# Kernel optimization log

Measured on AMD Instinct MI355X. Metric: run time of the kernel, lower is better.

The kernel has to match this reference:

```python
import jax, jax.numpy as jnp
import numpy as np

NEG_SLOPE = 0.2
EPS = 1e-5


def seg_softmax(e, idx, n):
    # numerically stable segment softmax over segments given by idx
    m = jax.ops.segment_max(e, idx, num_segments=n)
    ex = jnp.exp(e - m[idx])
    s = jax.ops.segment_sum(ex, idx, num_segments=n)
    return ex / (s[idx] + 1e-16)


def seg_mean(v, idx, n):
    s = jax.ops.segment_sum(v, idx, num_segments=n)
    cnt = jax.ops.segment_sum(jnp.ones((v.shape[0],), v.dtype), idx, num_segments=n)
    return s / jnp.maximum(cnt, 1.0)[:, None]


def setup_inputs() -> dict:
    key = jax.random.key(0)
    ks = jax.random.split(key, 20)
    N, E, C, H, G, L = 50000, 400000, 128, 4, 64, 4
    HC, MID = H * C, C * (H // 2)
    s = 0.05
    inp = {
        "x": jax.random.normal(ks[0], (N, C), jnp.float32),
        "edge_index": jax.random.randint(ks[1], (2, E), 0, N),
        "instr_vectors": jax.random.normal(ks[2], (L, G, C), jnp.float32),
        "global_language_feats": jax.random.normal(ks[3], (G, C), jnp.float32),
        "edge_attr": jax.random.normal(ks[4], (E, C), jnp.float32),
        "batch": jnp.sort(jax.random.randint(ks[5], (N,), 0, G)),
        # per-layer GATv2 conv params
        "Wl": s * jax.random.normal(ks[6], (L, C, HC), jnp.float32),
        "Wr": s * jax.random.normal(ks[7], (L, C, HC), jnp.float32),
        "We": s * jax.random.normal(ks[8], (L, C, HC), jnp.float32),
        "att": s * jax.random.normal(ks[9], (L, H, C), jnp.float32),
        # instruction-conditioned node-mask projection
        "Wm": s * jax.random.normal(ks[10], (L, C, C), jnp.float32),
        # x_proj MLP
        "p1_w": s * jax.random.normal(ks[11], (L, HC, MID), jnp.float32),
        "p1_b": jnp.zeros((L, MID), jnp.float32),
        "p2_w": s * jax.random.normal(ks[12], (L, MID, C), jnp.float32),
        "p2_b": jnp.zeros((L, C), jnp.float32),
        # GraphNorm params
        "gn_gamma": jnp.ones((L, C), jnp.float32),
        "gn_beta": jnp.zeros((L, C), jnp.float32),
        "gn_alpha": jnp.ones((L, C), jnp.float32),
    }
    return inp


def reference(x, edge_index, instr_vectors, global_language_feats, edge_attr, batch,
              Wl, Wr, We, att, Wm, p1_w, p1_b, p2_w, p2_b, gn_gamma, gn_beta, gn_alpha):
    N, C = x.shape
    L, G, _ = instr_vectors.shape
    H = att.shape[1]
    src, dst = edge_index[0], edge_index[1]
    inv_sqrt_c = 1.0 / jnp.sqrt(jnp.asarray(C, x.dtype))
    h = x
    for i in range(L):
        instr = instr_vectors[i]  # [G, C]
        # instruction-conditioned soft node mask (interpretable_mode)
        mask = jax.nn.sigmoid(jnp.sum((h @ Wm[i]) * instr[batch], axis=-1, keepdims=True) * inv_sqrt_c)  # [N,1]
        x_in = mask * h
        # GATv2 conv with edge features, heads concatenated
        xl = (x_in @ Wl[i]).reshape(N, H, C)
        xr = (x_in @ Wr[i]).reshape(N, H, C)
        ea = (edge_attr @ We[i]).reshape(-1, H, C)
        m = jax.nn.leaky_relu(xl[src] + xr[dst] + ea, NEG_SLOPE)           # [E,H,C]
        e = jnp.einsum('ehc,hc->eh', m, att[i])                            # [E,H]
        alpha = seg_softmax(e, dst, N)                                     # [E,H]
        out = jax.ops.segment_sum(alpha[:, :, None] * xl[src], dst, num_segments=N)  # [N,H,C]
        out = out.reshape(N, H * C)
        # x_proj MLP
        cr = jax.nn.gelu(out @ p1_w[i] + p1_b[i])
        cr = jax.nn.gelu(cr @ p2_w[i] + p2_b[i])                           # [N,C]
        # scatter scaled-dot-product attention: instruction query gates nodes per graph
        s = jnp.sum(instr[batch] * cr, axis=-1) * inv_sqrt_c               # [N]
        a = seg_softmax(s, batch, G)                                       # [N]
        cr = a[:, None] * cr
        # GraphNorm per graph
        mean = seg_mean(cr, batch, G)                                      # [G,C]
        sub = cr - gn_alpha[i] * mean[batch]
        var = seg_mean(sub * sub, batch, G)                                # [G,C]
        cr = gn_gamma[i] * sub / jnp.sqrt(var[batch] + EPS) + gn_beta[i]
        # residual + interpretable mask gating
        h = mask * (cr + h)
    return h
```

## Files before the change

kernel.cpp:

```cpp
#include <hip/hip_runtime.h>
#include <math.h>

#define CDIV(a,b) (((a)+(b)-1)/(b))

static constexpr int Cc   = 128;
static constexpr int Hh   = 4;
static constexpr int HCc  = 512;
static constexpr int MIDc = 256;
static constexpr float INV_SQRT_C = 0.08838834764831845f;

typedef __attribute__((ext_vector_type(8))) short bf16x8;
typedef __attribute__((ext_vector_type(4))) float f32x4;

__device__ __forceinline__ unsigned short f2bf(float f) {
    unsigned u = __float_as_uint(f);
    unsigned r = (u + 0x7FFFu + ((u >> 16) & 1u)) >> 16;
    return (unsigned short)r;
}
__device__ __forceinline__ float bf2f(unsigned short v) {
    return __uint_as_float(((unsigned)v) << 16);
}

__device__ __forceinline__ float gelu_tanh(float x) {
    float x3 = x * x * x;
    float t = tanhf(0.7978845608028654f * (x + 0.044715f * x3));
    return 0.5f * x * (1.0f + t);
}

__global__ void k_init_gb(int* gbeg, int* gend, int N, int G) {
    int g = blockIdx.x * blockDim.x + threadIdx.x;
    if (g < G) { gbeg[g] = N; gend[g] = 0; }
}

__global__ void k_node_bounds(const int* __restrict__ batch, int* gbeg, int* gend, int N) {
    int n = blockIdx.x * blockDim.x + threadIdx.x;
    if (n < N) { int b = batch[n]; atomicMin(&gbeg[b], n); atomicMax(&gend[b], n + 1); }
}

__global__ void k_hist(const int* __restrict__ dst, int* __restrict__ cnt, int E) {
    int e = blockIdx.x * blockDim.x + threadIdx.x;
    if (e < E) atomicAdd(&cnt[dst[e]], 1);
}

__global__ void k_scan_blocks(const int* __restrict__ cnt, int* __restrict__ excl,
                              int* __restrict__ partials, int N) {
    __shared__ int buf[1024];
    int tid = threadIdx.x;
    int i = blockIdx.x * 1024 + tid;
    int v = (i < N) ? cnt[i] : 0;
    buf[tid] = v; __syncthreads();
    for (int off = 1; off < 1024; off <<= 1) {
        int t = (tid >= off) ? buf[tid - off] : 0;
        __syncthreads();
        buf[tid] += t;
        __syncthreads();
    }
    if (i < N) excl[i] = buf[tid] - v;
    if (tid == 1023) partials[blockIdx.x] = buf[1023];
}

__global__ void k_scan_partials(int* partials, int P) {
    __shared__ int buf[1024];
    int tid = threadIdx.x;
    int v = (tid < P) ? partials[tid] : 0;
    buf[tid] = v; __syncthreads();
    for (int off = 1; off < 1024; off <<= 1) {
        int t = (tid >= off) ? buf[tid - off] : 0;
        __syncthreads();
        buf[tid] += t;
        __syncthreads();
    }
    if (tid < P) partials[tid] = buf[tid] - v;
}

__global__ void k_scan_add(int* __restrict__ rowoff, const int* __restrict__ partials, int N, int E) {
    int i = blockIdx.x * 1024 + threadIdx.x;
    if (i < N) rowoff[i] += partials[blockIdx.x];
    if (i == 0) rowoff[N] = E;
}

__global__ void k_scatter(const int* __restrict__ src, const int* __restrict__ dst,
                          const int* __restrict__ rowoff, int* __restrict__ cursor,
                          int* __restrict__ srcs, int* __restrict__ dsts,
                          int* __restrict__ eids, int E) {
    int e = blockIdx.x * blockDim.x + threadIdx.x;
    if (e < E) {
        int d = dst[e];
        int p = rowoff[d] + atomicAdd(&cursor[d], 1);
        srcs[p] = src[e];
        dsts[p] = d;
        eids[p] = e;
    }
}

__global__ void k_conv_ea(const float* __restrict__ edge_attr, const int* __restrict__ eids,
                          unsigned short* __restrict__ eaT, int E) {
    int idx = blockIdx.x * blockDim.x + threadIdx.x;
    if (idx >= E * 32) return;
    int p = idx >> 5, j = idx & 31;
    int eid = eids[p];
    float4 v = *(const float4*)(edge_attr + (size_t)eid * Cc + j * 4);
    unsigned short o[4] = {f2bf(v.x), f2bf(v.y), f2bf(v.z), f2bf(v.w)};
    *(ushort4*)(eaT + (size_t)p * Cc + j * 4) = *(ushort4*)o;
}

__global__ void k_w2bf_t(const float* __restrict__ W, unsigned short* __restrict__ Wt,
                         int K, int N, int lgK) {
    int total = K * N;
    const float* Wl = W + (size_t)blockIdx.y * total;
    unsigned short* Wo = Wt + (size_t)blockIdx.y * total;
    int idx = blockIdx.x * blockDim.x + threadIdx.x;
    if (idx >= total) return;
    int k = idx & (K - 1);
    int n = idx >> lgK;
    Wo[idx] = f2bf(Wl[(size_t)k * N + n]);
}

__global__ void k_compute_q(const float* __restrict__ Wm, const float* __restrict__ instr,
                            float* __restrict__ q, int G) {
    int idx = blockIdx.x * blockDim.x + threadIdx.x;
    if (idx >= G * Cc) return;
    int g = idx >> 7, k = idx & 127;
    const float* wrow = Wm + (size_t)k * Cc;
    const float* irow = instr + (size_t)g * Cc;
    float acc = 0.f;
    #pragma unroll 8
    for (int j = 0; j < Cc; ++j) acc += wrow[j] * irow[j];
    q[idx] = acc;
}

__global__ __launch_bounds__(256) void k_mask_xin(const float* __restrict__ h,
                                                  const float* __restrict__ q,
                                                  const int* __restrict__ batch,
                                                  float* __restrict__ maskv,
                                                  unsigned short* __restrict__ x_in, int N) {
    int wid = (blockIdx.x * blockDim.x + threadIdx.x) >> 6;
    if (wid >= N) return;
    int lane = threadIdx.x & 63;
    int b = batch[wid];
    float2 hv = ((const float2*)(h + (size_t)wid * Cc))[lane];
    float2 qv = ((const float2*)(q + (size_t)b * Cc))[lane];
    float part = hv.x * qv.x + hv.y * qv.y;
    #pragma unroll
    for (int off = 1; off < 64; off <<= 1) part += __shfl_xor(part, off);
    float m = 1.0f / (1.0f + expf(-part * INV_SQRT_C));
    if (lane == 0) maskv[wid] = m;
    unsigned short o[2] = {f2bf(m * hv.x), f2bf(m * hv.y)};
    *(ushort2*)(x_in + (size_t)wid * Cc + lane * 2) = *(ushort2*)o;
}

__global__ __launch_bounds__(256) void k_sdot(const float* __restrict__ cr,
                                              const float* __restrict__ instr,
                                              const int* __restrict__ batch,
                                              float* __restrict__ sarr, int N) {
    int wid = (blockIdx.x * blockDim.x + threadIdx.x) >> 6;
    if (wid >= N) return;
    int lane = threadIdx.x & 63;
    int b = batch[wid];
    float2 cv = ((const float2*)(cr + (size_t)wid * Cc))[lane];
    float2 iv = ((const float2*)(instr + (size_t)b * Cc))[lane];
    float part = cv.x * iv.x + cv.y * iv.y;
    #pragma unroll
    for (int off = 1; off < 64; off <<= 1) part += __shfl_xor(part, off);
    if (lane == 0) sarr[wid] = part * INV_SQRT_C;
}

__global__ __launch_bounds__(256) void k_gemm_bf16(const unsigned short* __restrict__ A,
                                                   const unsigned short* __restrict__ Bt,
                                                   const float* __restrict__ bias,
                                                   float* __restrict__ outF,
                                                   unsigned short* __restrict__ outB,
                                                   int M, int K, int N, int act) {
    int wave = threadIdx.x >> 6, lane = threadIdx.x & 63;
    int q = lane >> 4, l15 = lane & 15;
    int waves_per_n = N >> 7;
    int rows_per_block = (waves_per_n == 4) ? 32 : (waves_per_n == 2) ? 64 : 128;
    int wrow = (waves_per_n == 4) ? 0 : (waves_per_n == 2) ? (wave >> 1) : wave;
    int wcol = wave & (waves_per_n - 1);
    int r0 = blockIdx.x * rows_per_block + wrow * 32;
    int cb = wcol << 7;

    int ra = r0 + l15;        if (ra >= M) ra = M - 1;
    int rb = r0 + 16 + l15;   if (rb >= M) rb = M - 1;
    const unsigned short* Apa = A + (size_t)ra * K + q * 8;
    const unsigned short* Apb = A + (size_t)rb * K + q * 8;

    f32x4 acc[2][8] = {};
    for (int k0 = 0; k0 < K; k0 += 32) {
        bf16x8 a0 = *(const bf16x8*)(Apa + k0);
        bf16x8 a1 = *(const bf16x8*)(Apb + k0);
        #pragma unroll
        for (int t = 0; t < 8; ++t) {
            int n = cb + t * 16 + l15;
            bf16x8 b = *(const bf16x8*)(Bt + (size_t)n * K + k0 + q * 8);
            acc[0][t] = __builtin_amdgcn_mfma_f32_16x16x32_bf16(a0, b, acc[0][t], 0, 0, 0);
            acc[1][t] = __builtin_amdgcn_mfma_f32_16x16x32_bf16(a1, b, acc[1][t], 0, 0, 0);
        }
    }
    #pragma unroll
    for (int s = 0; s < 2; ++s) {
        #pragma unroll
        for (int t = 0; t < 8; ++t) {
            int n = cb + t * 16 + l15;
            float bv = bias ? bias[n] : 0.f;
            #pragma unroll
            for (int r = 0; r < 4; ++r) {
                int m = r0 + s * 16 + q * 4 + r;
                if (m < M) {
                    float v = acc[s][t][r] + bv;
                    if (act) v = gelu_tanh(v);
                    if (outF) outF[(size_t)m * N + n] = v;
                    if (outB) outB[(size_t)m * N + n] = f2bf(v);
                }
            }
        }
    }
}

__global__ __launch_bounds__(256) void k_edge_scores_mfma(const unsigned short* __restrict__ eaT,
                                                          const unsigned short* __restrict__ WeT,
                                                          const float* __restrict__ xl,
                                                          const unsigned short* __restrict__ xr,
                                                          const int* __restrict__ srcs,
                                                          const int* __restrict__ dsts,
                                                          const float* __restrict__ att,
                                                          float* __restrict__ scores, int E) {
    int wave = threadIdx.x >> 6, lane = threadIdx.x & 63;
    int q = lane >> 4, l15 = lane & 15;
    int p0 = blockIdx.x * 32;
    __shared__ int s_src[32], s_dst[32];
    if (threadIdx.x < 32) {
        int p = p0 + threadIdx.x;
        int pc = (p < E) ? p : E - 1;
        s_src[threadIdx.x] = srcs[pc];
        s_dst[threadIdx.x] = dsts[pc];
    }
    __syncthreads();

    int h = wave;
    int cbh = h << 7;
    int e0 = p0 + l15;      if (e0 >= E) e0 = E - 1;
    int e1 = p0 + 16 + l15; if (e1 >= E) e1 = E - 1;
    const unsigned short* Ap0 = eaT + (size_t)e0 * Cc + q * 8;
    const unsigned short* Ap1 = eaT + (size_t)e1 * Cc + q * 8;

    f32x4 acc[2][8] = {};
    #pragma unroll
    for (int k0 = 0; k0 < 128; k0 += 32) {
        bf16x8 a0 = *(const bf16x8*)(Ap0 + k0);
        bf16x8 a1 = *(const bf16x8*)(Ap1 + k0);
        #pragma unroll
        for (int t = 0; t < 8; ++t) {
            int n = cbh + t * 16 + l15;
            bf16x8 b = *(const bf16x8*)(WeT + (size_t)n * Cc + k0 + q * 8);
            acc[0][t] = __builtin_amdgcn_mfma_f32_16x16x32_bf16(a0, b, acc[0][t], 0, 0, 0);
            acc[1][t] = __builtin_amdgcn_mfma_f32_16x16x32_bf16(a1, b, acc[1][t], 0, 0, 0);
        }
    }

    float sc[2][4] = {{0.f,0.f,0.f,0.f},{0.f,0.f,0.f,0.f}};
    #pragma unroll
    for (int t = 0; t < 8; ++t) {
        int n = cbh + t * 16 + l15;
        float attn = att[n];
        #pragma unroll
        for (int s = 0; s < 2; ++s) {
            #pragma unroll
            for (int r = 0; r < 4; ++r) {
                int ei = s * 16 + q * 4 + r;
                int sN = s_src[ei], dN = s_dst[ei];
                float v = acc[s][t][r] + xl[(size_t)sN * HCc + n] + bf2f(xr[(size_t)dN * HCc + n]);
                v = (v > 0.f) ? v : 0.2f * v;
                sc[s][r] += v * attn;
            }
        }
    }
    #pragma unroll
    for (int s = 0; s < 2; ++s) {
        #pragma unroll
        for (int r = 0; r < 4; ++r) {
            float v = sc[s][r];
            v += __shfl_xor(v, 1);
            v += __shfl_xor(v, 2);
            v += __shfl_xor(v, 4);
            v += __shfl_xor(v, 8);
            if (l15 == 0) {
                int p = p0 + s * 16 + q * 4 + r;
                if (p < E) scores[(size_t)p * 4 + h] = v;
            }
        }
    }
}

__global__ __launch_bounds__(256) void k_edge_agg(const float* __restrict__ xl,
                                                  const float* __restrict__ scores,
                                                  const int* __restrict__ rowoff,
                                                  const int* __restrict__ srcs,
                                                  unsigned short* __restrict__ out, int N) {
    int wid = (blockIdx.x * blockDim.x + threadIdx.x) >> 6;
    if (wid >= N) return;
    int lane = threadIdx.x & 63;
    int cbase = lane << 3;
    int h = lane >> 4;

    float m_run = -INFINITY, s_run = 0.f;
    float acc[8] = {0.f, 0.f, 0.f, 0.f, 0.f, 0.f, 0.f, 0.f};

    int p0 = rowoff[wid], p1 = rowoff[wid + 1];
    for (int p = p0; p < p1; ++p) {
        int s = srcs[p];
        float sc_e = scores[(size_t)p * 4 + h];
        float4 l0 = *(const float4*)(xl + (size_t)s * HCc + cbase);
        float4 l1 = *(const float4*)(xl + (size_t)s * HCc + cbase + 4);
        float xlv[8] = {l0.x, l0.y, l0.z, l0.w, l1.x, l1.y, l1.z, l1.w};
        float mn = fmaxf(m_run, sc_e);
        float rescale = expf(m_run - mn);
        float w = expf(sc_e - mn);
        s_run = s_run * rescale + w;
        #pragma unroll
        for (int j = 0; j < 8; ++j) acc[j] = acc[j] * rescale + w * xlv[j];
        m_run = mn;
    }
    float inv = 1.0f / (s_run + 1e-16f);
    unsigned short o[8];
    #pragma unroll
    for (int j = 0; j < 8; ++j) o[j] = f2bf(acc[j] * inv);
    *(bf16x8*)(out + (size_t)wid * HCc + cbase) = *(bf16x8*)o;
}

__global__ void k_graph_softmax(const float* __restrict__ s, const int* __restrict__ gbeg,
                                const int* __restrict__ gend, float* __restrict__ a) {
    int g = blockIdx.x;
    int n0 = gbeg[g], n1 = gend[g];
    __shared__ float red[256];
    int tid = threadIdx.x;
    float lm = -INFINITY;
    for (int n = n0 + tid; n < n1; n += 256) lm = fmaxf(lm, s[n]);
    red[tid] = lm; __syncthreads();
    for (int off = 128; off > 0; off >>= 1) {
        if (tid < off) red[tid] = fmaxf(red[tid], red[tid + off]);
        __syncthreads();
    }
    float mx = red[0]; __syncthreads();
    float ls = 0.f;
    for (int n = n0 + tid; n < n1; n += 256) ls += expf(s[n] - mx);
    red[tid] = ls; __syncthreads();
    for (int off = 128; off > 0; off >>= 1) {
        if (tid < off) red[tid] += red[tid + off];
        __syncthreads();
    }
    float inv = 1.0f / (red[0] + 1e-16f);
    for (int n = n0 + tid; n < n1; n += 256) a[n] = expf(s[n] - mx) * inv;
}

__global__ __launch_bounds__(512) void k_gn_stats(const float* __restrict__ cr,
                                                  const float* __restrict__ a,
                                                  const int* __restrict__ gbeg,
                                                  const int* __restrict__ gend,
                                                  const float* __restrict__ alpha,
                                                  float* __restrict__ meanb,
                                                  float* __restrict__ varb) {
    int g = blockIdx.x;
    int n0 = gbeg[g], n1 = gend[g];
    int c = threadIdx.x & 127;
    int sub = threadIdx.x >> 7;
    __shared__ float red[4][128];
    float accv = 0.f;
    for (int n = n0 + sub; n < n1; n += 4) accv += a[n] * cr[(size_t)n * Cc + c];
    red[sub][c] = accv; __syncthreads();
    float cntf = (n1 > n0) ? (float)(n1 - n0) : 0.f;
    float invc = 1.0f / fmaxf(cntf, 1.0f);
    if (sub == 0) {
        float m = (red[0][c] + red[1][c] + red[2][c] + red[3][c]) * invc;
        meanb[g * Cc + c] = m;
        red[0][c] = m;
    }
    __syncthreads();
    float mean = red[0][c];
    __syncthreads();
    float am = alpha[c] * mean;
    float acc2 = 0.f;
    for (int n = n0 + sub; n < n1; n += 4) {
        float v = a[n] * cr[(size_t)n * Cc + c] - am;
        acc2 += v * v;
    }
    red[sub][c] = acc2; __syncthreads();
    if (sub == 0) varb[g * Cc + c] = (red[0][c] + red[1][c] + red[2][c] + red[3][c]) * invc;
}

__global__ void k_final(const float* __restrict__ cr, const float* __restrict__ a,
                        const float* __restrict__ h, const float* __restrict__ maskv,
                        const int* __restrict__ batch, const float* __restrict__ meanb,
                        const float* __restrict__ varb, const float* __restrict__ gamma,
                        const float* __restrict__ beta, const float* __restrict__ alpha,
                        float* __restrict__ hout, int N) {
    int idx = blockIdx.x * blockDim.x + threadIdx.x;
    if (idx >= N * Cc) return;
    int n = idx >> 7, c = idx & 127;
    int g = batch[n];
    float acr = a[n] * cr[idx];
    float sb = acr - alpha[c] * meanb[g * Cc + c];
    float crn = gamma[c] * sb / sqrtf(varb[g * Cc + c] + 1e-5f) + beta[c];
    hout[idx] = maskv[n] * (crn + h[idx]);
}

extern "C" void kernel_launch(void* const* d_in, const int* in_sizes, int n_in,
                              void* d_out, int out_size, void* d_ws, size_t ws_size,
                              hipStream_t stream) {
    const float* x         = (const float*)d_in[0];
    const int*   edge_idx  = (const int*)d_in[1];
    const float* instr     = (const float*)d_in[2];
    const float* edge_attr = (const float*)d_in[4];
    const int*   batch     = (const int*)d_in[5];
    const float* Wl        = (const float*)d_in[6];
    const float* Wr        = (const float*)d_in[7];
    const float* We        = (const float*)d_in[8];
    const float* att       = (const float*)d_in[9];
    const float* Wm        = (const float*)d_in[10];
    const float* p1_w      = (const float*)d_in[11];
    const float* p1_b      = (const float*)d_in[12];
    const float* p2_w      = (const float*)d_in[13];
    const float* p2_b      = (const float*)d_in[14];
    const float* gn_gamma  = (const float*)d_in[15];
    const float* gn_beta   = (const float*)d_in[16];
    const float* gn_alpha  = (const float*)d_in[17];

    const int N = in_sizes[0] / Cc;
    const int E = in_sizes[4] / Cc;
    const int G = in_sizes[3] / Cc;
    const int L = in_sizes[6] / (Cc * HCc);
    (void)n_in; (void)ws_size; (void)out_size;

    const int* e_src = edge_idx;
    const int* e_dst = edge_idx + E;

    char* pw = (char*)d_ws;
    auto alloc = [&](size_t bytes) -> void* {
        void* r = (void*)pw;
        pw += (bytes + 255) & ~(size_t)255;
        return r;
    };
    float* h_buf            = (float*)alloc((size_t)N * Cc * 4);
    void*  xin_cr_region    = alloc((size_t)N * Cc * 4);
    float* xl               = (float*)alloc((size_t)N * HCc * 4);
    unsigned short* xr      = (unsigned short*)alloc((size_t)N * HCc * 2);
    unsigned short* aggB    = (unsigned short*)alloc((size_t)N * HCc * 2);
    unsigned short* eaT     = (unsigned short*)alloc((size_t)E * Cc * 2);
    float* scores           = (float*)alloc((size_t)E * 4 * 4);
    unsigned short* WlT     = (unsigned short*)alloc((size_t)L * Cc * HCc * 2);
    unsigned short* WrT     = (unsigned short*)alloc((size_t)L * Cc * HCc * 2);
    unsigned short* WeT     = (unsigned short*)alloc((size_t)L * Cc * HCc * 2);
    unsigned short* p1T     = (unsigned short*)alloc((size_t)L * HCc * MIDc * 2);
    unsigned short* p2T     = (unsigned short*)alloc((size_t)L * MIDc * Cc * 2);
    float* maskv  = (float*)alloc((size_t)N * 4);
    float* sarr   = (float*)alloc((size_t)N * 4);
    float* aarr   = (float*)alloc((size_t)N * 4);
    float* qbuf   = (float*)alloc((size_t)G * Cc * 4);
    float* meanb  = (float*)alloc((size_t)G * Cc * 4);
    float* varb   = (float*)alloc((size_t)G * Cc * 4);
    int* rowoff   = (int*)alloc(((size_t)N + 1) * 4);
    int* cnt      = (int*)alloc((size_t)N * 4);
    int* cursor   = (int*)alloc((size_t)N * 4);
    int* gbeg     = (int*)alloc((size_t)G * 4);
    int* gend     = (int*)alloc((size_t)G * 4);
    int* partials = (int*)alloc(1024 * 4);
    int* srcs     = (int*)alloc((size_t)E * 4);
    int* dsts     = (int*)alloc((size_t)E * 4);
    int* eids     = (int*)alloc((size_t)E * 4);
    unsigned short* x_in = (unsigned short*)xin_cr_region;
    float* cr            = (float*)xin_cr_region;
    unsigned short* mid  = xr;

    hipMemcpyAsync(h_buf, x, (size_t)N * Cc * 4, hipMemcpyDeviceToDevice, stream);

    k_init_gb<<<CDIV(G, 64), 64, 0, stream>>>(gbeg, gend, N, G);
    k_node_bounds<<<CDIV(N, 256), 256, 0, stream>>>(batch, gbeg, gend, N);

    hipMemsetAsync(cnt, 0, (size_t)N * 4, stream);
    hipMemsetAsync(cursor, 0, (size_t)N * 4, stream);
    k_hist<<<CDIV(E, 256), 256, 0, stream>>>(e_dst, cnt, E);
    int nb = CDIV(N, 1024);
    k_scan_blocks<<<nb, 1024, 0, stream>>>(cnt, rowoff, partials, N);
    k_scan_partials<<<1, 1024, 0, stream>>>(partials, nb);
    k_scan_add<<<nb, 1024, 0, stream>>>(rowoff, partials, N, E);
    k_scatter<<<CDIV(E, 256), 256, 0, stream>>>(e_src, e_dst, rowoff, cursor, srcs, dsts, eids, E);

    k_conv_ea<<<CDIV(E * 32, 256), 256, 0, stream>>>(edge_attr, eids, eaT, E);
    {
        dim3 g1(CDIV(Cc * HCc, 256), L);
        k_w2bf_t<<<g1, 256, 0, stream>>>(Wl, WlT, Cc, HCc, 7);
        k_w2bf_t<<<g1, 256, 0, stream>>>(Wr, WrT, Cc, HCc, 7);
        k_w2bf_t<<<g1, 256, 0, stream>>>(We, WeT, Cc, HCc, 7);
        dim3 g2(CDIV(HCc * MIDc, 256), L);
        k_w2bf_t<<<g2, 256, 0, stream>>>(p1_w, p1T, HCc, MIDc, 9);
        dim3 g3(CDIV(MIDc * Cc, 256), L);
        k_w2bf_t<<<g3, 256, 0, stream>>>(p2_w, p2T, MIDc, Cc, 8);
    }

    for (int i = 0; i < L; ++i) {
        const float* Wm_i    = Wm + (size_t)i * Cc * Cc;
        const float* instr_i = instr + (size_t)i * G * Cc;
        const unsigned short* WlT_i = WlT + (size_t)i * Cc * HCc;
        const unsigned short* WrT_i = WrT + (size_t)i * Cc * HCc;
        const unsigned short* WeT_i = WeT + (size_t)i * Cc * HCc;
        const unsigned short* p1T_i = p1T + (size_t)i * HCc * MIDc;
        const unsigned short* p2T_i = p2T + (size_t)i * MIDc * Cc;
        const float* att_i   = att + (size_t)i * Hh * Cc;
        const float* p1b_i   = p1_b + (size_t)i * MIDc;
        const float* p2b_i   = p2_b + (size_t)i * Cc;
        const float* gam_i   = gn_gamma + (size_t)i * Cc;
        const float* bet_i   = gn_beta + (size_t)i * Cc;
        const float* alp_i   = gn_alpha + (size_t)i * Cc;

        k_compute_q<<<CDIV(G * Cc, 256), 256, 0, stream>>>(Wm_i, instr_i, qbuf, G);
        k_mask_xin<<<CDIV(N, 4), 256, 0, stream>>>(h_buf, qbuf, batch, maskv, x_in, N);

        k_gemm_bf16<<<CDIV(N, 32), 256, 0, stream>>>(x_in, WlT_i, nullptr, xl, nullptr, N, Cc, HCc, 0);
        k_gemm_bf16<<<CDIV(N, 32), 256, 0, stream>>>(x_in, WrT_i, nullptr, nullptr, xr, N, Cc, HCc, 0);

        k_edge_scores_mfma<<<CDIV(E, 32), 256, 0, stream>>>(eaT, WeT_i, xl, xr, srcs, dsts,
                                                            att_i, scores, E);
        k_edge_agg<<<CDIV(N, 4), 256, 0, stream>>>(xl, scores, rowoff, srcs, aggB, N);

        k_gemm_bf16<<<CDIV(N, 64), 256, 0, stream>>>(aggB, p1T_i, p1b_i, nullptr, mid, N, HCc, MIDc, 1);
        k_gemm_bf16<<<CDIV(N, 128), 256, 0, stream>>>(mid, p2T_i, p2b_i, cr, nullptr, N, MIDc, Cc, 1);

        k_sdot<<<CDIV(N, 4), 256, 0, stream>>>(cr, instr_i, batch, sarr, N);
        k_graph_softmax<<<G, 256, 0, stream>>>(sarr, gbeg, gend, aarr);

        k_gn_stats<<<G, 512, 0, stream>>>(cr, aarr, gbeg, gend, alp_i, meanb, varb);

        float* hout = (i == L - 1) ? (float*)d_out : h_buf;
        k_final<<<CDIV(N * Cc, 256), 256, 0, stream>>>(cr, aarr, h_buf, maskv, batch, meanb,
                                                       varb, gam_i, bet_i, alp_i, hout, N);
    }
}
```

Before: 4.458 ms.

## Fuse xl/xr projections into edge-score GEMM via concatenated K=384 weights

The edge-score kernel now computes ea·We + x_src·Wl + x_dst·Wr in a single MFMA loop over a concatenated K=384 weight matrix, gathering the bf16 x_in rows of each edge's endpoints. This removes the separate Wr GEMM and the per-edge random gathers of 512-wide xl/xr rows in the scoring epilogue. xl is now stored only in bf16 for aggregation, which halves gather traffic in k_edge_agg at some precision cost. The trade-off is three times more MFMA work per edge (E is 8x N), in exchange for much less gather traffic.

```diff
diff --git a/kernel.cpp b/kernel.cpp
--- a/kernel.cpp
+++ b/kernel.cpp
@@ -7,6 +7,7 @@
 static constexpr int Hh   = 4;
 static constexpr int HCc  = 512;
 static constexpr int MIDc = 256;
+static constexpr int KS   = 384;
 static constexpr float INV_SQRT_C = 0.08838834764831845f;
 
 typedef __attribute__((ext_vector_type(8))) short bf16x8;
@@ -114,6 +115,20 @@
     int k = idx & (K - 1);
     int n = idx >> lgK;
     Wo[idx] = f2bf(Wl[(size_t)k * N + n]);
+}
+
+__global__ void k_build_bst(const float* __restrict__ We, const float* __restrict__ Wl,
+                            const float* __restrict__ Wr, unsigned short* __restrict__ BtS) {
+    int l = blockIdx.y;
+    int idx = blockIdx.x * blockDim.x + threadIdx.x;
+    if (idx >= HCc * KS) return;
+    int n = idx / KS, k = idx - n * KS;
+    size_t woff = (size_t)l * Cc * HCc;
+    float v;
+    if (k < 128)      v = We[woff + (size_t)k * HCc + n];
+    else if (k < 256) v = Wl[woff + (size_t)(k - 128) * HCc + n];
+    else              v = Wr[woff + (size_t)(k - 256) * HCc + n];
+    BtS[(size_t)l * HCc * KS + idx] = f2bf(v);
 }
 
 __global__ void k_compute_q(const float* __restrict__ Wm, const float* __restrict__ instr,
@@ -217,14 +232,13 @@
     }
 }
 
-__global__ __launch_bounds__(256) void k_edge_scores_mfma(const unsigned short* __restrict__ eaT,
-                                                          const unsigned short* __restrict__ WeT,
-                                                          const float* __restrict__ xl,
-                                                          const unsigned short* __restrict__ xr,
-                                                          const int* __restrict__ srcs,
-                                                          const int* __restrict__ dsts,
-                                                          const float* __restrict__ att,
-                                                          float* __restrict__ scores, int E) {
+__global__ __launch_bounds__(256) void k_edge_scores_fused(const unsigned short* __restrict__ eaT,
+                                                           const unsigned short* __restrict__ x_in,
+                                                           const unsigned short* __restrict__ BtS,
+                                                           const int* __restrict__ srcs,
+                                                           const int* __restrict__ dsts,
+                                                           const float* __restrict__ att,
+                                                           float* __restrict__ scores, int E) {
     int wave = threadIdx.x >> 6, lane = threadIdx.x & 63;
     int q = lane >> 4, l15 = lane & 15;
     int p0 = blockIdx.x * 32;
@@ -239,20 +253,28 @@
 
     int h = wave;
     int cbh = h << 7;
-    int e0 = p0 + l15;      if (e0 >= E) e0 = E - 1;
-    int e1 = p0 + 16 + l15; if (e1 >= E) e1 = E - 1;
-    const unsigned short* Ap0 = eaT + (size_t)e0 * Cc + q * 8;
-    const unsigned short* Ap1 = eaT + (size_t)e1 * Cc + q * 8;
+    int eA = p0 + l15;      if (eA >= E) eA = E - 1;
+    int eB = p0 + 16 + l15; if (eB >= E) eB = E - 1;
+    const unsigned short* a_ea[2] = { eaT + (size_t)eA * Cc + q * 8,
+                                      eaT + (size_t)eB * Cc + q * 8 };
+    const unsigned short* a_xs[2] = { x_in + (size_t)s_src[l15] * Cc + q * 8,
+                                      x_in + (size_t)s_src[16 + l15] * Cc + q * 8 };
+    const unsigned short* a_xd[2] = { x_in + (size_t)s_dst[l15] * Cc + q * 8,
+                                      x_in + (size_t)s_dst[16 + l15] * Cc + q * 8 };
 
     f32x4 acc[2][8] = {};
     #pragma unroll
-    for (int k0 = 0; k0 < 128; k0 += 32) {
-        bf16x8 a0 = *(const bf16x8*)(Ap0 + k0);
-        bf16x8 a1 = *(const bf16x8*)(Ap1 + k0);
+    for (int c = 0; c < 12; ++c) {
+        int k0 = c << 5;
+        int koff = (c & 3) << 5;
+        bf16x8 a0, a1;
+        if (c < 4)      { a0 = *(const bf16x8*)(a_ea[0] + koff); a1 = *(const bf16x8*)(a_ea[1] + koff); }
+        else if (c < 8) { a0 = *(const bf16x8*)(a_xs[0] + koff); a1 = *(const bf16x8*)(a_xs[1] + koff); }
+        else            { a0 = *(const bf16x8*)(a_xd[0] + koff); a1 = *(const bf16x8*)(a_xd[1] + koff); }
         #pragma unroll
         for (int t = 0; t < 8; ++t) {
             int n = cbh + t * 16 + l15;
-            bf16x8 b = *(const bf16x8*)(WeT + (size_t)n * Cc + k0 + q * 8);
+            bf16x8 b = *(const bf16x8*)(BtS + (size_t)n * KS + k0 + q * 8);
             acc[0][t] = __builtin_amdgcn_mfma_f32_16x16x32_bf16(a0, b, acc[0][t], 0, 0, 0);
             acc[1][t] = __builtin_amdgcn_mfma_f32_16x16x32_bf16(a1, b, acc[1][t], 0, 0, 0);
         }
@@ -267,9 +289,7 @@
         for (int s = 0; s < 2; ++s) {
             #pragma unroll
             for (int r = 0; r < 4; ++r) {
-                int ei = s * 16 + q * 4 + r;
-                int sN = s_src[ei], dN = s_dst[ei];
-                float v = acc[s][t][r] + xl[(size_t)sN * HCc + n] + bf2f(xr[(size_t)dN * HCc + n]);
+                float v = acc[s][t][r];
                 v = (v > 0.f) ? v : 0.2f * v;
                 sc[s][r] += v * attn;
             }
@@ -292,7 +312,7 @@
     }
 }
 
-__global__ __launch_bounds__(256) void k_edge_agg(const float* __restrict__ xl,
+__global__ __launch_bounds__(256) void k_edge_agg(const unsigned short* __restrict__ xlB,
                                                   const float* __restrict__ scores,
                                                   const int* __restrict__ rowoff,
                                                   const int* __restrict__ srcs,
@@ -310,9 +330,10 @@
     for (int p = p0; p < p1; ++p) {
         int s = srcs[p];
         float sc_e = scores[(size_t)p * 4 + h];
-        float4 l0 = *(const float4*)(xl + (size_t)s * HCc + cbase);
-        float4 l1 = *(const float4*)(xl + (size_t)s * HCc + cbase + 4);
-        float xlv[8] = {l0.x, l0.y, l0.z, l0.w, l1.x, l1.y, l1.z, l1.w};
+        ushort4 u0 = *(const ushort4*)(xlB + (size_t)s * HCc + cbase);
+        ushort4 u1 = *(const ushort4*)(xlB + (size_t)s * HCc + cbase + 4);
+        float xlv[8] = {bf2f(u0.x), bf2f(u0.y), bf2f(u0.z), bf2f(u0.w),
+                        bf2f(u1.x), bf2f(u1.y), bf2f(u1.z), bf2f(u1.w)};
         float mn = fmaxf(m_run, sc_e);
         float rescale = expf(m_run - mn);
         float w = expf(sc_e - mn);
@@ -442,14 +463,13 @@
     };
     float* h_buf            = (float*)alloc((size_t)N * Cc * 4);
     void*  xin_cr_region    = alloc((size_t)N * Cc * 4);
-    float* xl               = (float*)alloc((size_t)N * HCc * 4);
-    unsigned short* xr      = (unsigned short*)alloc((size_t)N * HCc * 2);
+    unsigned short* xlB     = (unsigned short*)alloc((size_t)N * HCc * 2);
     unsigned short* aggB    = (unsigned short*)alloc((size_t)N * HCc * 2);
+    unsigned short* mid     = (unsigned short*)alloc((size_t)N * MIDc * 2);
     unsigned short* eaT     = (unsigned short*)alloc((size_t)E * Cc * 2);
     float* scores           = (float*)alloc((size_t)E * 4 * 4);
     unsigned short* WlT     = (unsigned short*)alloc((size_t)L * Cc * HCc * 2);
-    unsigned short* WrT     = (unsigned short*)alloc((size_t)L * Cc * HCc * 2);
-    unsigned short* WeT     = (unsigned short*)alloc((size_t)L * Cc * HCc * 2);
+    unsigned short* BtS     = (unsigned short*)alloc((size_t)L * HCc * KS * 2);
     unsigned short* p1T     = (unsigned short*)alloc((size_t)L * HCc * MIDc * 2);
     unsigned short* p2T     = (unsigned short*)alloc((size_t)L * MIDc * Cc * 2);
     float* maskv  = (float*)alloc((size_t)N * 4);
@@ -469,7 +489,6 @@
     int* eids     = (int*)alloc((size_t)E * 4);
     unsigned short* x_in = (unsigned short*)xin_cr_region;
     float* cr            = (float*)xin_cr_region;
-    unsigned short* mid  = xr;
 
     hipMemcpyAsync(h_buf, x, (size_t)N * Cc * 4, hipMemcpyDeviceToDevice, stream);
 
@@ -489,8 +508,8 @@
     {
         dim3 g1(CDIV(Cc * HCc, 256), L);
         k_w2bf_t<<<g1, 256, 0, stream>>>(Wl, WlT, Cc, HCc, 7);
-        k_w2bf_t<<<g1, 256, 0, stream>>>(Wr, WrT, Cc, HCc, 7);
-        k_w2bf_t<<<g1, 256, 0, stream>>>(We, WeT, Cc, HCc, 7);
+        dim3 gs(CDIV(HCc * KS, 256), L);
+        k_build_bst<<<gs, 256, 0, stream>>>(We, Wl, Wr, BtS);
         dim3 g2(CDIV(HCc * MIDc, 256), L);
         k_w2bf_t<<<g2, 256, 0, stream>>>(p1_w, p1T, HCc, MIDc, 9);
         dim3 g3(CDIV(MIDc * Cc, 256), L);
@@ -501,8 +520,7 @@
         const float* Wm_i    = Wm + (size_t)i * Cc * Cc;
         const float* instr_i = instr + (size_t)i * G * Cc;
         const unsigned short* WlT_i = WlT + (size_t)i * Cc * HCc;
-        const unsigned short* WrT_i = WrT + (size_t)i * Cc * HCc;
-        const unsigned short* WeT_i = WeT + (size_t)i * Cc * HCc;
+        const unsigned short* BtS_i = BtS + (size_t)i * HCc * KS;
         const unsigned short* p1T_i = p1T + (size_t)i * HCc * MIDc;
         const unsigned short* p2T_i = p2T + (size_t)i * MIDc * Cc;
         const float* att_i   = att + (size_t)i * Hh * Cc;
@@ -515,12 +533,11 @@
         k_compute_q<<<CDIV(G * Cc, 256), 256, 0, stream>>>(Wm_i, instr_i, qbuf, G);
         k_mask_xin<<<CDIV(N, 4), 256, 0, stream>>>(h_buf, qbuf, batch, maskv, x_in, N);
 
-        k_gemm_bf16<<<CDIV(N, 32), 256, 0, stream>>>(x_in, WlT_i, nullptr, xl, nullptr, N, Cc, HCc, 0);
-        k_gemm_bf16<<<CDIV(N, 32), 256, 0, stream>>>(x_in, WrT_i, nullptr, nullptr, xr, N, Cc, HCc, 0);
-
-        k_edge_scores_mfma<<<CDIV(E, 32), 256, 0, stream>>>(eaT, WeT_i, xl, xr, srcs, dsts,
-                                                            att_i, scores, E);
-        k_edge_agg<<<CDIV(N, 4), 256, 0, stream>>>(xl, scores, rowoff, srcs, aggB, N);
+        k_gemm_bf16<<<CDIV(N, 32), 256, 0, stream>>>(x_in, WlT_i, nullptr, nullptr, xlB, N, Cc, HCc, 0);
+
+        k_edge_scores_fused<<<CDIV(E, 32), 256, 0, stream>>>(eaT, x_in, BtS_i, srcs, dsts,
+                                                             att_i, scores, E);
+        k_edge_agg<<<CDIV(N, 4), 256, 0, stream>>>(xlB, scores, rowoff, srcs, aggB, N);
 
         k_gemm_bf16<<<CDIV(N, 64), 256, 0, stream>>>(aggB, p1T_i, p1b_i, nullptr, mid, N, HCc, MIDc, 1);
         k_gemm_bf16<<<CDIV(N, 128), 256, 0, stream>>>(mid, p2T_i, p2b_i, cr, nullptr, N, MIDc, Cc, 1);
```

After: 5.079 ms. 13.9% more time.

## Fuse edge scoring into aggregation with precomputed bf16 edge projections

Applied to the files above, without the earlier changes.

The per-edge score kernel is removed. Edge-attribute projections are now precomputed by the generic GEMM into a bf16 E×512 buffer, and a single per-destination wave kernel computes the leaky-ReLU attention score, the online softmax and the weighted aggregation together, prefetching the next edge's data. xl is stored in bf16 rather than fp32, which halves its gather traffic and drops the dsts array and the scores round trip. In exchange it writes and reads a large 400k×512 bf16 projection buffer per layer and adds bf16 rounding to xl.

```diff
diff --git a/kernel.cpp b/kernel.cpp
--- a/kernel.cpp
+++ b/kernel.cpp
@@ -81,14 +81,12 @@
 
 __global__ void k_scatter(const int* __restrict__ src, const int* __restrict__ dst,
                           const int* __restrict__ rowoff, int* __restrict__ cursor,
-                          int* __restrict__ srcs, int* __restrict__ dsts,
-                          int* __restrict__ eids, int E) {
+                          int* __restrict__ srcs, int* __restrict__ eids, int E) {
     int e = blockIdx.x * blockDim.x + threadIdx.x;
     if (e < E) {
         int d = dst[e];
         int p = rowoff[d] + atomicAdd(&cursor[d], 1);
         srcs[p] = src[e];
-        dsts[p] = d;
         eids[p] = e;
     }
 }
@@ -217,109 +215,63 @@
     }
 }
 
-__global__ __launch_bounds__(256) void k_edge_scores_mfma(const unsigned short* __restrict__ eaT,
-                                                          const unsigned short* __restrict__ WeT,
-                                                          const float* __restrict__ xl,
-                                                          const unsigned short* __restrict__ xr,
-                                                          const int* __restrict__ srcs,
-                                                          const int* __restrict__ dsts,
-                                                          const float* __restrict__ att,
-                                                          float* __restrict__ scores, int E) {
-    int wave = threadIdx.x >> 6, lane = threadIdx.x & 63;
-    int q = lane >> 4, l15 = lane & 15;
-    int p0 = blockIdx.x * 32;
-    __shared__ int s_src[32], s_dst[32];
-    if (threadIdx.x < 32) {
-        int p = p0 + threadIdx.x;
-        int pc = (p < E) ? p : E - 1;
-        s_src[threadIdx.x] = srcs[pc];
-        s_dst[threadIdx.x] = dsts[pc];
-    }
-    __syncthreads();
-
-    int h = wave;
-    int cbh = h << 7;
-    int e0 = p0 + l15;      if (e0 >= E) e0 = E - 1;
-    int e1 = p0 + 16 + l15; if (e1 >= E) e1 = E - 1;
-    const unsigned short* Ap0 = eaT + (size_t)e0 * Cc + q * 8;
-    const unsigned short* Ap1 = eaT + (size_t)e1 * Cc + q * 8;
-
-    f32x4 acc[2][8] = {};
-    #pragma unroll
-    for (int k0 = 0; k0 < 128; k0 += 32) {
-        bf16x8 a0 = *(const bf16x8*)(Ap0 + k0);
-        bf16x8 a1 = *(const bf16x8*)(Ap1 + k0);
-        #pragma unroll
-        for (int t = 0; t < 8; ++t) {
-            int n = cbh + t * 16 + l15;
-            bf16x8 b = *(const bf16x8*)(WeT + (size_t)n * Cc + k0 + q * 8);
-            acc[0][t] = __builtin_amdgcn_mfma_f32_16x16x32_bf16(a0, b, acc[0][t], 0, 0, 0);
-            acc[1][t] = __builtin_amdgcn_mfma_f32_16x16x32_bf16(a1, b, acc[1][t], 0, 0, 0);
-        }
-    }
-
-    float sc[2][4] = {{0.f,0.f,0.f,0.f},{0.f,0.f,0.f,0.f}};
-    #pragma unroll
-    for (int t = 0; t < 8; ++t) {
-        int n = cbh + t * 16 + l15;
-        float attn = att[n];
-        #pragma unroll
-        for (int s = 0; s < 2; ++s) {
-            #pragma unroll
-            for (int r = 0; r < 4; ++r) {
-                int ei = s * 16 + q * 4 + r;
-                int sN = s_src[ei], dN = s_dst[ei];
-                float v = acc[s][t][r] + xl[(size_t)sN * HCc + n] + bf2f(xr[(size_t)dN * HCc + n]);
-                v = (v > 0.f) ? v : 0.2f * v;
-                sc[s][r] += v * attn;
-            }
-        }
-    }
-    #pragma unroll
-    for (int s = 0; s < 2; ++s) {
-        #pragma unroll
-        for (int r = 0; r < 4; ++r) {
-            float v = sc[s][r];
-            v += __shfl_xor(v, 1);
-            v += __shfl_xor(v, 2);
-            v += __shfl_xor(v, 4);
-            v += __shfl_xor(v, 8);
-            if (l15 == 0) {
-                int p = p0 + s * 16 + q * 4 + r;
-                if (p < E) scores[(size_t)p * 4 + h] = v;
-            }
-        }
-    }
-}
-
-__global__ __launch_bounds__(256) void k_edge_agg(const float* __restrict__ xl,
-                                                  const float* __restrict__ scores,
-                                                  const int* __restrict__ rowoff,
-                                                  const int* __restrict__ srcs,
-                                                  unsigned short* __restrict__ out, int N) {
+__global__ __launch_bounds__(256) void k_edge_fused(const unsigned short* __restrict__ eaP,
+                                                    const unsigned short* __restrict__ xlB,
+                                                    const unsigned short* __restrict__ xrB,
+                                                    const float* __restrict__ att,
+                                                    const int* __restrict__ rowoff,
+                                                    const int* __restrict__ srcs,
+                                                    unsigned short* __restrict__ out, int N) {
     int wid = (blockIdx.x * blockDim.x + threadIdx.x) >> 6;
     if (wid >= N) return;
     int lane = threadIdx.x & 63;
     int cbase = lane << 3;
-    int h = lane >> 4;
+
+    bf16x8 rv = *(const bf16x8*)(xrB + (size_t)wid * HCc + cbase);
+    float xrv[8];
+    #pragma unroll
+    for (int j = 0; j < 8; ++j) xrv[j] = bf2f((unsigned short)rv[j]);
+    float4 a0 = *(const float4*)(att + cbase);
+    float4 a1 = *(const float4*)(att + cbase + 4);
+    float attv[8] = {a0.x, a0.y, a0.z, a0.w, a1.x, a1.y, a1.z, a1.w};
 
     float m_run = -INFINITY, s_run = 0.f;
     float acc[8] = {0.f, 0.f, 0.f, 0.f, 0.f, 0.f, 0.f, 0.f};
 
     int p0 = rowoff[wid], p1 = rowoff[wid + 1];
+    bf16x8 ea_c = {}, xl_c = {};
+    if (p0 < p1) {
+        ea_c = *(const bf16x8*)(eaP + (size_t)p0 * HCc + cbase);
+        xl_c = *(const bf16x8*)(xlB + (size_t)srcs[p0] * HCc + cbase);
+    }
     for (int p = p0; p < p1; ++p) {
-        int s = srcs[p];
-        float sc_e = scores[(size_t)p * 4 + h];
-        float4 l0 = *(const float4*)(xl + (size_t)s * HCc + cbase);
-        float4 l1 = *(const float4*)(xl + (size_t)s * HCc + cbase + 4);
-        float xlv[8] = {l0.x, l0.y, l0.z, l0.w, l1.x, l1.y, l1.z, l1.w};
-        float mn = fmaxf(m_run, sc_e);
+        bf16x8 ea_n = ea_c, xl_n = xl_c;
+        if (p + 1 < p1) {
+            ea_n = *(const bf16x8*)(eaP + (size_t)(p + 1) * HCc + cbase);
+            xl_n = *(const bf16x8*)(xlB + (size_t)srcs[p + 1] * HCc + cbase);
+        }
+        float xlv[8], part = 0.f;
+        #pragma unroll
+        for (int j = 0; j < 8; ++j) {
+            float eaf = bf2f((unsigned short)ea_c[j]);
+            float xlf = bf2f((unsigned short)xl_c[j]);
+            xlv[j] = xlf;
+            float z = eaf + xlf + xrv[j];
+            z = (z > 0.f) ? z : 0.2f * z;
+            part = fmaf(z, attv[j], part);
+        }
+        part += __shfl_xor(part, 1);
+        part += __shfl_xor(part, 2);
+        part += __shfl_xor(part, 4);
+        part += __shfl_xor(part, 8);
+        float mn = fmaxf(m_run, part);
         float rescale = expf(m_run - mn);
-        float w = expf(sc_e - mn);
+        float w = expf(part - mn);
         s_run = s_run * rescale + w;
         #pragma unroll
-        for (int j = 0; j < 8; ++j) acc[j] = acc[j] * rescale + w * xlv[j];
+        for (int j = 0; j < 8; ++j) acc[j] = fmaf(w, xlv[j], acc[j] * rescale);
         m_run = mn;
+        ea_c = ea_n; xl_c = xl_n;
     }
     float inv = 1.0f / (s_run + 1e-16f);
     unsigned short o[8];
@@ -442,11 +394,12 @@
     };
     float* h_buf            = (float*)alloc((size_t)N * Cc * 4);
     void*  xin_cr_region    = alloc((size_t)N * Cc * 4);
-    float* xl               = (float*)alloc((size_t)N * HCc * 4);
-    unsigned short* xr      = (unsigned short*)alloc((size_t)N * HCc * 2);
+    unsigned short* xlB     = (unsigned short*)alloc((size_t)N * HCc * 2);
+    unsigned short* xrB     = (unsigned short*)alloc((size_t)N * HCc * 2);
     unsigned short* aggB    = (unsigned short*)alloc((size_t)N * HCc * 2);
+    unsigned short* mid     = (unsigned short*)alloc((size_t)N * MIDc * 2);
     unsigned short* eaT     = (unsigned short*)alloc((size_t)E * Cc * 2);
-    float* scores           = (float*)alloc((size_t)E * 4 * 4);
+    unsigned short* eaP     = (unsigned short*)alloc((size_t)E * HCc * 2);
     unsigned short* WlT     = (unsigned short*)alloc((size_t)L * Cc * HCc * 2);
     unsigned short* WrT     = (unsigned short*)alloc((size_t)L * Cc * HCc * 2);
     unsigned short* WeT     = (unsigned short*)alloc((size_t)L * Cc * HCc * 2);
@@ -465,11 +418,9 @@
     int* gend     = (int*)alloc((size_t)G * 4);
     int* partials = (int*)alloc(1024 * 4);
     int* srcs     = (int*)alloc((size_t)E * 4);
-    int* dsts     = (int*)alloc((size_t)E * 4);
     int* eids     = (int*)alloc((size_t)E * 4);
     unsigned short* x_in = (unsigned short*)xin_cr_region;
     float* cr            = (float*)xin_cr_region;
-    unsigned short* mid  = xr;
 
     hipMemcpyAsync(h_buf, x, (size_t)N * Cc * 4, hipMemcpyDeviceToDevice, stream);
 
@@ -483,7 +434,7 @@
     k_scan_blocks<<<nb, 1024, 0, stream>>>(cnt, rowoff, partials, N);
     k_scan_partials<<<1, 1024, 0, stream>>>(partials, nb);
     k_scan_add<<<nb, 1024, 0, stream>>>(rowoff, partials, N, E);
-    k_scatter<<<CDIV(E, 256), 256, 0, stream>>>(e_src, e_dst, rowoff, cursor, srcs, dsts, eids, E);
+    k_scatter<<<CDIV(E, 256), 256, 0, stream>>>(e_src, e_dst, rowoff, cursor, srcs, eids, E);
 
     k_conv_ea<<<CDIV(E * 32, 256), 256, 0, stream>>>(edge_attr, eids, eaT, E);
     {
@@ -515,12 +466,12 @@
         k_compute_q<<<CDIV(G * Cc, 256), 256, 0, stream>>>(Wm_i, instr_i, qbuf, G);
         k_mask_xin<<<CDIV(N, 4), 256, 0, stream>>>(h_buf, qbuf, batch, maskv, x_in, N);
 
-        k_gemm_bf16<<<CDIV(N, 32), 256, 0, stream>>>(x_in, WlT_i, nullptr, xl, nullptr, N, Cc, HCc, 0);
-        k_gemm_bf16<<<CDIV(N, 32), 256, 0, stream>>>(x_in, WrT_i, nullptr, nullptr, xr, N, Cc, HCc, 0);
-
-        k_edge_scores_mfma<<<CDIV(E, 32), 256, 0, stream>>>(eaT, WeT_i, xl, xr, srcs, dsts,
-                                                            att_i, scores, E);
-        k_edge_agg<<<CDIV(N, 4), 256, 0, stream>>>(xl, scores, rowoff, srcs, aggB, N);
+        k_gemm_bf16<<<CDIV(N, 32), 256, 0, stream>>>(x_in, WlT_i, nullptr, nullptr, xlB, N, Cc, HCc, 0);
+        k_gemm_bf16<<<CDIV(N, 32), 256, 0, stream>>>(x_in, WrT_i, nullptr, nullptr, xrB, N, Cc, HCc, 0);
+
+        k_gemm_bf16<<<CDIV(E, 32), 256, 0, stream>>>(eaT, WeT_i, nullptr, nullptr, eaP, E, Cc, HCc, 0);
+
+        k_edge_fused<<<CDIV(N, 4), 256, 0, stream>>>(eaP, xlB, xrB, att_i, rowoff, srcs, aggB, N);
 
         k_gemm_bf16<<<CDIV(N, 64), 256, 0, stream>>>(aggB, p1T_i, p1b_i, nullptr, mid, N, HCc, MIDc, 1);
         k_gemm_bf16<<<CDIV(N, 128), 256, 0, stream>>>(mid, p2T_i, p2b_i, cr, nullptr, N, MIDc, Cc, 1);
```

Result: no change. 4.472 ms (+0.3%).
